# Optimization experiments

Measured on AMD Instinct MI355X. Metric: run time of the kernel, lower is better.

Reference implementation:

```python
import jax, jax.numpy as jnp
import numpy as np

EPS = 1e-05


def setup_inputs() -> dict:
    key = jax.random.key(0)
    kx, kw, kb, kg, kp, kq = jax.random.split(key, 6)
    B, S, D = 32, 1024, 1024
    x = jax.random.normal(kx, (B, S, D), dtype=jnp.float32)
    # Linear(input_size, input_size) params
    W = jax.random.normal(kw, (D, D), dtype=jnp.float32) / np.sqrt(D)
    b = jax.random.normal(kb, (D,), dtype=jnp.float32) * 0.01
    gold_opinion = jax.random.uniform(kg, (B, S, 5), dtype=jnp.float32)
    predict_opinion = jax.random.uniform(kp, (B, S, 5), dtype=jnp.float32)
    gold_prob = jax.random.uniform(kq, (), dtype=jnp.float32)
    return {"x": x, "W": W, "b": b, "gold_opinion": gold_opinion,
            "predict_opinion": predict_opinion, "gold_prob": gold_prob}


def reference(x, W, b, gold_opinion, predict_opinion, gold_prob):
    # x: [B, S, D]
    S = x.shape[-2]
    x_tran = jnp.einsum('bsd,ed->bse', x, W) + b           # Linear: x @ W^T + b
    weights = jnp.einsum('bsd,btd->bst', x_tran, x)        # QK^T -> [B, S, S]

    idx = jnp.arange(S)
    location = jnp.abs(idx[None, :] - idx[:, None]).astype(x.dtype)  # [S, S]
    weights = weights * (1.0 / (location + EPS))           # distance decay

    # use_opinion = True branch
    gold_op = gold_opinion[:, :, 1] + gold_opinion[:, :, 2]          # [B, S]
    pred_op = predict_opinion[:, :, 3] + predict_opinion[:, :, 4]    # [B, S]
    opinion_weights = gold_prob * gold_op + (1.0 - gold_prob) * pred_op
    weights = weights * opinion_weights[:, :, None]

    weights = jnp.exp(jnp.tanh(weights))                   # pseudo-softmax numerator
    off_diag = (location != 0).astype(weights.dtype)       # eye(S) == 0 mask
    weights = weights * off_diag
    weights = weights / (jnp.sum(weights, axis=-1, keepdims=True) + EPS)
    return jnp.einsum('bst,btd->bsd', weights, x)
```

## Files before the change

### kernel.cpp

```cpp
#include <hip/hip_runtime.h>

#define EPSF 1e-5f

typedef _Float16 f16x8 __attribute__((ext_vector_type(8)));
typedef float f32x4 __attribute__((ext_vector_type(4)));

__device__ __forceinline__ void gload_lds16(const _Float16* g, _Float16* l) {
  __builtin_amdgcn_global_load_lds(
      (const __attribute__((address_space(1))) unsigned int*)g,
      (__attribute__((address_space(3))) unsigned int*)l, 16, 0, 0);
}

__device__ __forceinline__ f16x8 cvt8(float4 a, float4 b) {
  f16x8 h;
  h[0] = (_Float16)a.x; h[1] = (_Float16)a.y; h[2] = (_Float16)a.z; h[3] = (_Float16)a.w;
  h[4] = (_Float16)b.x; h[5] = (_Float16)b.y; h[6] = (_Float16)b.z; h[7] = (_Float16)b.w;
  return h;
}

__global__ void prep_opin_k(const float* __restrict__ gold, const float* __restrict__ pred,
                            const float* __restrict__ gprob, float* __restrict__ opin, int n) {
  int i = blockIdx.x * 256 + threadIdx.x;
  if (i >= n) return;
  float gp = gprob[0];
  float go = gold[i * 5 + 1] + gold[i * 5 + 2];
  float po = pred[i * 5 + 3] + pred[i * 5 + 4];
  opin[i] = gp * go + (1.0f - gp) * po;
}

__global__ __launch_bounds__(256) void prep_h_k(const float* __restrict__ src,
                                                _Float16* __restrict__ dst) {
  long i = ((long)blockIdx.x * 256 + threadIdx.x) * 8;
  float4 a = *(const float4*)(src + i);
  float4 b = *(const float4*)(src + i + 4);
  *(f16x8*)(dst + i) = cvt8(a, b);
}

__global__ __launch_bounds__(256) void prep_xt_k(const float* __restrict__ x,
                                                 _Float16* __restrict__ XhT) {
  const int d = blockIdx.x * 256 + threadIdx.x;
  const int ts = blockIdx.y * 64;
  const long base = (long)blockIdx.z * 1024;
#pragma unroll
  for (int tg = 0; tg < 4; ++tg) {
    int t0 = ts + tg * 16;
    const float* src = x + (base + t0) * 1024 + d;
    float v[16];
#pragma unroll
    for (int j = 0; j < 16; ++j) v[j] = src[j * 1024];
    f16x8 h0, h1;
#pragma unroll
    for (int j = 0; j < 8; ++j) { h0[j] = (_Float16)v[j]; h1[j] = (_Float16)v[8 + j]; }
    _Float16* dst = XhT + (base + d) * 1024 + t0;
    *(f16x8*)dst = h0;
    *(f16x8*)(dst + 8) = h1;
  }
}

__global__ __launch_bounds__(256) void gemm1_h_k(const _Float16* __restrict__ Xh,
                                                 const _Float16* __restrict__ Wh,
                                                 const float* __restrict__ bias,
                                                 _Float16* __restrict__ XT) {
  __shared__ _Float16 As[128 * 32];
  __shared__ _Float16 Bs[128 * 32];
  const int tid = threadIdx.x;
  const int wave = tid >> 6, lane = tid & 63;
  const int wm = wave >> 1, wn = wave & 1;
  const int quad = lane >> 4, nl = lane & 15;
  const long m0 = (long)blockIdx.y * 128;
  const int n0 = blockIdx.x * 128;

  f32x4 acc[4][4];
  f32x4 zero = {0.f, 0.f, 0.f, 0.f};
#pragma unroll
  for (int i = 0; i < 4; ++i)
#pragma unroll
    for (int j = 0; j < 4; ++j) acc[i][j] = zero;

  for (int k0 = 0; k0 < 1024; k0 += 32) {
#pragma unroll
    for (int it = 0; it < 2; ++it) {
      int c = it * 256 + tid;
      gload_lds16(Xh + (m0 + (c >> 2)) * 1024 + k0 + (c & 3) * 8,
                  &As[(it * 256 + wave * 64) * 8]);
      gload_lds16(Wh + (long)(n0 + (c >> 2)) * 1024 + k0 + (c & 3) * 8,
                  &Bs[(it * 256 + wave * 64) * 8]);
    }
    __syncthreads();
    f16x8 af[4], bf[4];
#pragma unroll
    for (int mi = 0; mi < 4; ++mi)
      af[mi] = *(const f16x8*)&As[(wm * 64 + mi * 16 + nl) * 32 + quad * 8];
#pragma unroll
    for (int ni = 0; ni < 4; ++ni)
      bf[ni] = *(const f16x8*)&Bs[(wn * 64 + ni * 16 + nl) * 32 + quad * 8];
#pragma unroll
    for (int mi = 0; mi < 4; ++mi)
#pragma unroll
      for (int ni = 0; ni < 4; ++ni)
        acc[mi][ni] = __builtin_amdgcn_mfma_f32_16x16x32_f16(af[mi], bf[ni], acc[mi][ni], 0, 0, 0);
    __syncthreads();
  }

#pragma unroll
  for (int mi = 0; mi < 4; ++mi) {
    long gm = m0 + wm * 64 + mi * 16 + quad * 4;
#pragma unroll
    for (int ni = 0; ni < 4; ++ni) {
      int gn = n0 + wn * 64 + ni * 16 + nl;
      float bv = bias[gn];
#pragma unroll
      for (int r = 0; r < 4; ++r)
        XT[(gm + r) * 1024 + gn] = (_Float16)(acc[mi][ni][r] + bv);
    }
  }
}

__global__ __launch_bounds__(256) void gemm1_k(const _Float16* __restrict__ Xh,
                                               const float* __restrict__ Wt,
                                               const float* __restrict__ bias,
                                               _Float16* __restrict__ XT) {
  __shared__ _Float16 As[128 * 32];
  __shared__ _Float16 Bs[128 * 32];
  const int tid = threadIdx.x;
  const int wave = tid >> 6, lane = tid & 63;
  const int wm = wave >> 1, wn = wave & 1;
  const int quad = lane >> 4, nl = lane & 15;
  const long m0 = (long)blockIdx.y * 128;
  const int n0 = blockIdx.x * 128;

  f32x4 acc[4][4];
  f32x4 zero = {0.f, 0.f, 0.f, 0.f};
#pragma unroll
  for (int i = 0; i < 4; ++i)
#pragma unroll
    for (int j = 0; j < 4; ++j) acc[i][j] = zero;

  const int crow = tid >> 2;
  const int ckc = (tid & 3) * 8;

  for (int k0 = 0; k0 < 1024; k0 += 32) {
#pragma unroll
    for (int it = 0; it < 2; ++it) {
      int c = it * 256 + tid;
      gload_lds16(Xh + (m0 + (c >> 2)) * 1024 + k0 + (c & 3) * 8,
                  &As[(it * 256 + wave * 64) * 8]);
      int row = it * 64 + crow;
      const float* sb = Wt + (long)(n0 + row) * 1024 + k0 + ckc;
      float4 b0 = *(const float4*)sb;
      float4 b1 = *(const float4*)(sb + 4);
      *(f16x8*)&Bs[row * 32 + ckc] = cvt8(b0, b1);
    }
    __syncthreads();
    f16x8 af[4], bf[4];
#pragma unroll
    for (int mi = 0; mi < 4; ++mi)
      af[mi] = *(const f16x8*)&As[(wm * 64 + mi * 16 + nl) * 32 + quad * 8];
#pragma unroll
    for (int ni = 0; ni < 4; ++ni)
      bf[ni] = *(const f16x8*)&Bs[(wn * 64 + ni * 16 + nl) * 32 + quad * 8];
#pragma unroll
    for (int mi = 0; mi < 4; ++mi)
#pragma unroll
      for (int ni = 0; ni < 4; ++ni)
        acc[mi][ni] = __builtin_amdgcn_mfma_f32_16x16x32_f16(af[mi], bf[ni], acc[mi][ni], 0, 0, 0);
    __syncthreads();
  }

#pragma unroll
  for (int mi = 0; mi < 4; ++mi) {
    long gm = m0 + wm * 64 + mi * 16 + quad * 4;
#pragma unroll
    for (int ni = 0; ni < 4; ++ni) {
      int gn = n0 + wn * 64 + ni * 16 + nl;
      float bv = bias[gn];
#pragma unroll
      for (int r = 0; r < 4; ++r)
        XT[(gm + r) * 1024 + gn] = (_Float16)(acc[mi][ni][r] + bv);
    }
  }
}

__global__ __launch_bounds__(256) void scores_k(const _Float16* __restrict__ XT,
                                                const _Float16* __restrict__ Xh,
                                                const float* __restrict__ opin,
                                                _Float16* __restrict__ P,
                                                float* __restrict__ denom) {
  __shared__ _Float16 As[128 * 32];
  __shared__ _Float16 Bs[128 * 32];
  const int tid = threadIdx.x;
  const int wave = tid >> 6, lane = tid & 63;
  const int wm = wave >> 1, wn = wave & 1;
  const int quad = lane >> 4, nl = lane & 15;

  const int lin = blockIdx.x;
  const int xcd = lin & 7;
  const int i = lin >> 3;
  const int b = xcd + 8 * (i >> 6);
  const int tile = i & 63;
  const int s0 = (tile >> 3) * 128;
  const int t0 = (tile & 7) * 128;
  const long base = (long)b * 1024;

  f32x4 acc[4][4];
  f32x4 zero = {0.f, 0.f, 0.f, 0.f};
#pragma unroll
  for (int i2 = 0; i2 < 4; ++i2)
#pragma unroll
    for (int j = 0; j < 4; ++j) acc[i2][j] = zero;

  for (int k0 = 0; k0 < 1024; k0 += 32) {
#pragma unroll
    for (int it = 0; it < 2; ++it) {
      int c = it * 256 + tid;
      gload_lds16(XT + (base + s0 + (c >> 2)) * 1024 + k0 + (c & 3) * 8,
                  &As[(it * 256 + wave * 64) * 8]);
      gload_lds16(Xh + (base + t0 + (c >> 2)) * 1024 + k0 + (c & 3) * 8,
                  &Bs[(it * 256 + wave * 64) * 8]);
    }
    __syncthreads();
    f16x8 af[4], bf[4];
#pragma unroll
    for (int mi = 0; mi < 4; ++mi)
      af[mi] = *(const f16x8*)&As[(wm * 64 + mi * 16 + nl) * 32 + quad * 8];
#pragma unroll
    for (int ni = 0; ni < 4; ++ni)
      bf[ni] = *(const f16x8*)&Bs[(wn * 64 + ni * 16 + nl) * 32 + quad * 8];
#pragma unroll
    for (int mi = 0; mi < 4; ++mi)
#pragma unroll
      for (int ni = 0; ni < 4; ++ni)
        acc[mi][ni] = __builtin_amdgcn_mfma_f32_16x16x32_f16(af[mi], bf[ni], acc[mi][ni], 0, 0, 0);
    __syncthreads();
  }

#pragma unroll
  for (int mi = 0; mi < 4; ++mi) {
#pragma unroll
    for (int r = 0; r < 4; ++r) {
      int s = s0 + wm * 64 + mi * 16 + quad * 4 + r;
      float opv = opin[b * 1024 + s];
      float rs = 0.f;
#pragma unroll
      for (int ni = 0; ni < 4; ++ni) {
        int t = t0 + wn * 64 + ni * 16 + nl;
        float loc = fabsf((float)(s - t));
        float arg = acc[mi][ni][r] * (1.0f / (loc + EPSF)) * opv;
        float th = 1.f - 2.f / (__expf(2.f * arg) + 1.f);
        float p = __expf(th);
        if (s == t) p = 0.f;
        P[(base + s) * 1024 + t] = (_Float16)p;
        rs += p;
      }
      rs += __shfl_xor(rs, 1);
      rs += __shfl_xor(rs, 2);
      rs += __shfl_xor(rs, 4);
      rs += __shfl_xor(rs, 8);
      if (nl == 0) atomicAdd(&denom[b * 1024 + s], rs);
    }
  }
}

__global__ __launch_bounds__(256) void pv_h_k(const _Float16* __restrict__ P,
                                              const _Float16* __restrict__ XhT,
                                              const float* __restrict__ denom,
                                              float* __restrict__ out) {
  __shared__ _Float16 As[128 * 32];
  __shared__ _Float16 Bs[128 * 32];
  const int tid = threadIdx.x;
  const int wave = tid >> 6, lane = tid & 63;
  const int wm = wave >> 1, wn = wave & 1;
  const int quad = lane >> 4, nl = lane & 15;

  const int lin = blockIdx.x;
  const int xcd = lin & 7;
  const int i = lin >> 3;
  const int b = xcd + 8 * (i >> 6);
  const int tile = i & 63;
  const int s0 = (tile >> 3) * 128;
  const int d0 = (tile & 7) * 128;
  const long base = (long)b * 1024;

  f32x4 acc[4][4];
  f32x4 zero = {0.f, 0.f, 0.f, 0.f};
#pragma unroll
  for (int i2 = 0; i2 < 4; ++i2)
#pragma unroll
    for (int j = 0; j < 4; ++j) acc[i2][j] = zero;

  for (int k0 = 0; k0 < 1024; k0 += 32) {
#pragma unroll
    for (int it = 0; it < 2; ++it) {
      int c = it * 256 + tid;
      gload_lds16(P + (base + s0 + (c >> 2)) * 1024 + k0 + (c & 3) * 8,
                  &As[(it * 256 + wave * 64) * 8]);
      gload_lds16(XhT + (base + d0 + (c >> 2)) * 1024 + k0 + (c & 3) * 8,
                  &Bs[(it * 256 + wave * 64) * 8]);
    }
    __syncthreads();
    f16x8 af[4], bf[4];
#pragma unroll
    for (int mi = 0; mi < 4; ++mi)
      af[mi] = *(const f16x8*)&As[(wm * 64 + mi * 16 + nl) * 32 + quad * 8];
#pragma unroll
    for (int ni = 0; ni < 4; ++ni)
      bf[ni] = *(const f16x8*)&Bs[(wn * 64 + ni * 16 + nl) * 32 + quad * 8];
#pragma unroll
    for (int mi = 0; mi < 4; ++mi)
#pragma unroll
      for (int ni = 0; ni < 4; ++ni)
        acc[mi][ni] = __builtin_amdgcn_mfma_f32_16x16x32_f16(af[mi], bf[ni], acc[mi][ni], 0, 0, 0);
    __syncthreads();
  }

#pragma unroll
  for (int mi = 0; mi < 4; ++mi) {
#pragma unroll
    for (int r = 0; r < 4; ++r) {
      int s = s0 + wm * 64 + mi * 16 + quad * 4 + r;
      float inv = 1.0f / (denom[b * 1024 + s] + EPSF);
#pragma unroll
      for (int ni = 0; ni < 4; ++ni) {
        int d = d0 + wn * 64 + ni * 16 + nl;
        out[(base + s) * 1024 + d] = acc[mi][ni][r] * inv;
      }
    }
  }
}

__global__ __launch_bounds__(256) void pv_k(const _Float16* __restrict__ P,
                                            const float* __restrict__ X,
                                            const float* __restrict__ denom,
                                            float* __restrict__ out) {
  __shared__ _Float16 As[128 * 32];
  __shared__ _Float16 BsT[128 * 40];
  const int tid = threadIdx.x;
  const int wave = tid >> 6, lane = tid & 63;
  const int wm = wave >> 1, wn = wave & 1;
  const int quad = lane >> 4, nl = lane & 15;
  const int b = blockIdx.z;
  const int s0 = blockIdx.y * 128;
  const int d0 = blockIdx.x * 128;
  const long base = (long)b * 1024;

  const int dcol = tid & 127;
  const int tg = tid >> 7;

  f32x4 acc[4][4];
  f32x4 zero = {0.f, 0.f, 0.f, 0.f};
#pragma unroll
  for (int i = 0; i < 4; ++i)
#pragma unroll
    for (int j = 0; j < 4; ++j) acc[i][j] = zero;

  for (int k0 = 0; k0 < 1024; k0 += 32) {
#pragma unroll
    for (int it = 0; it < 2; ++it) {
      int c = it * 256 + tid;
      gload_lds16(P + (base + s0 + (c >> 2)) * 1024 + k0 + (c & 3) * 8,
                  &As[(it * 256 + wave * 64) * 8]);
    }
    {
      const float* xb = X + (base + k0 + tg * 16) * 1024 + d0 + dcol;
      float v[16];
#pragma unroll
      for (int j = 0; j < 16; ++j) v[j] = xb[j * 1024];
      f16x8 h0, h1;
#pragma unroll
      for (int j = 0; j < 8; ++j) { h0[j] = (_Float16)v[j]; h1[j] = (_Float16)v[8 + j]; }
      *(f16x8*)&BsT[dcol * 40 + tg * 16] = h0;
      *(f16x8*)&BsT[dcol * 40 + tg * 16 + 8] = h1;
    }
    __syncthreads();
    f16x8 af[4], bf[4];
#pragma unroll
    for (int mi = 0; mi < 4; ++mi)
      af[mi] = *(const f16x8*)&As[(wm * 64 + mi * 16 + nl) * 32 + quad * 8];
#pragma unroll
    for (int ni = 0; ni < 4; ++ni)
      bf[ni] = *(const f16x8*)&BsT[(wn * 64 + ni * 16 + nl) * 40 + quad * 8];
#pragma unroll
    for (int mi = 0; mi < 4; ++mi)
#pragma unroll
      for (int ni = 0; ni < 4; ++ni)
        acc[mi][ni] = __builtin_amdgcn_mfma_f32_16x16x32_f16(af[mi], bf[ni], acc[mi][ni], 0, 0, 0);
    __syncthreads();
  }

#pragma unroll
  for (int mi = 0; mi < 4; ++mi) {
#pragma unroll
    for (int r = 0; r < 4; ++r) {
      int s = s0 + wm * 64 + mi * 16 + quad * 4 + r;
      float inv = 1.0f / (denom[b * 1024 + s] + EPSF);
#pragma unroll
      for (int ni = 0; ni < 4; ++ni) {
        int d = d0 + wn * 64 + ni * 16 + nl;
        out[(base + s) * 1024 + d] = acc[mi][ni][r] * inv;
      }
    }
  }
}

__global__ __launch_bounds__(256) void scores_f_k(const _Float16* __restrict__ XT,
                                                  const _Float16* __restrict__ Xh,
                                                  const float* __restrict__ opin,
                                                  _Float16* __restrict__ P,
                                                  float* __restrict__ denom) {
  __shared__ _Float16 As[128 * 32];
  __shared__ _Float16 Bs[128 * 32];
  const int tid = threadIdx.x;
  const int wave = tid >> 6, lane = tid & 63;
  const int wm = wave >> 1, wn = wave & 1;
  const int quad = lane >> 4, nl = lane & 15;
  const int b = blockIdx.z;
  const int s0 = blockIdx.y * 128;
  const int t0 = blockIdx.x * 128;
  const long base = (long)b * 1024;

  f32x4 acc[4][4];
  f32x4 zero = {0.f, 0.f, 0.f, 0.f};
#pragma unroll
  for (int i = 0; i < 4; ++i)
#pragma unroll
    for (int j = 0; j < 4; ++j) acc[i][j] = zero;

  for (int k0 = 0; k0 < 1024; k0 += 32) {
#pragma unroll
    for (int it = 0; it < 2; ++it) {
      int c = it * 256 + tid;
      gload_lds16(XT + (base + s0 + (c >> 2)) * 1024 + k0 + (c & 3) * 8,
                  &As[(it * 256 + wave * 64) * 8]);
      gload_lds16(Xh + (base + t0 + (c >> 2)) * 1024 + k0 + (c & 3) * 8,
                  &Bs[(it * 256 + wave * 64) * 8]);
    }
    __syncthreads();
    f16x8 af[4], bf[4];
#pragma unroll
    for (int mi = 0; mi < 4; ++mi)
      af[mi] = *(const f16x8*)&As[(wm * 64 + mi * 16 + nl) * 32 + quad * 8];
#pragma unroll
    for (int ni = 0; ni < 4; ++ni)
      bf[ni] = *(const f16x8*)&Bs[(wn * 64 + ni * 16 + nl) * 32 + quad * 8];
#pragma unroll
    for (int mi = 0; mi < 4; ++mi)
#pragma unroll
      for (int ni = 0; ni < 4; ++ni)
        acc[mi][ni] = __builtin_amdgcn_mfma_f32_16x16x32_f16(af[mi], bf[ni], acc[mi][ni], 0, 0, 0);
    __syncthreads();
  }

#pragma unroll
  for (int mi = 0; mi < 4; ++mi) {
#pragma unroll
    for (int r = 0; r < 4; ++r) {
      int s = s0 + wm * 64 + mi * 16 + quad * 4 + r;
      float opv = opin[b * 1024 + s];
      float rs = 0.f;
#pragma unroll
      for (int ni = 0; ni < 4; ++ni) {
        int t = t0 + wn * 64 + ni * 16 + nl;
        float loc = fabsf((float)(s - t));
        float arg = acc[mi][ni][r] * (1.0f / (loc + EPSF)) * opv;
        float th = 1.f - 2.f / (__expf(2.f * arg) + 1.f);
        float p = __expf(th);
        if (s == t) p = 0.f;
        P[(base + s) * 1024 + t] = (_Float16)p;
        rs += p;
      }
      rs += __shfl_xor(rs, 1);
      rs += __shfl_xor(rs, 2);
      rs += __shfl_xor(rs, 4);
      rs += __shfl_xor(rs, 8);
      if (nl == 0) atomicAdd(&denom[b * 1024 + s], rs);
    }
  }
}

extern "C" void kernel_launch(void* const* d_in, const int* in_sizes, int n_in,
                              void* d_out, int out_size, void* d_ws, size_t ws_size,
                              hipStream_t stream) {
  (void)in_sizes; (void)n_in; (void)out_size;
  const int B = 32, S = 1024;
  const int BS = B * S;

  const float* x     = (const float*)d_in[0];
  const float* W     = (const float*)d_in[1];
  const float* bias  = (const float*)d_in[2];
  const float* gold  = (const float*)d_in[3];
  const float* pred  = (const float*)d_in[4];
  const float* gprob = (const float*)d_in[5];

  const size_t P_BYTES  = (size_t)BS * 1024 * sizeof(_Float16);
  const size_t XT_BYTES = P_BYTES;
  const size_t OPIN_B   = (size_t)BS * sizeof(float);
  const size_t WH_B     = (size_t)1024 * 1024 * sizeof(_Float16);
  const size_t NEED_BIG = P_BYTES + XT_BYTES + 2 * OPIN_B + WH_B;

  char* ws = (char*)d_ws;
  _Float16* P = (_Float16*)ws;
  const bool big = ws_size >= NEED_BIG;

  _Float16* XT = (_Float16*)d_out;
  _Float16* Xh = XT + (size_t)BS * 1024;
  float* out   = (float*)d_out;

  if (big) {
    _Float16* XhT = (_Float16*)(ws + P_BYTES);
    float* opin   = (float*)(ws + P_BYTES + XT_BYTES);
    float* denom  = opin + BS;
    _Float16* Wh  = (_Float16*)(ws + P_BYTES + XT_BYTES + 2 * OPIN_B);

    hipMemsetAsync(denom, 0, OPIN_B, stream);
    prep_opin_k<<<BS / 256, 256, 0, stream>>>(gold, pred, gprob, opin, BS);
    prep_h_k<<<(BS * 1024 / 8) / 256, 256, 0, stream>>>(x, Xh);
    prep_h_k<<<(1024 * 1024 / 8) / 256, 256, 0, stream>>>(W, Wh);
    prep_xt_k<<<dim3(4, 16, 32), 256, 0, stream>>>(x, XhT);
    gemm1_h_k<<<dim3(8, 256), 256, 0, stream>>>(Xh, Wh, bias, XT);
    scores_k<<<2048, 256, 0, stream>>>(XT, Xh, opin, P, denom);
    pv_h_k<<<2048, 256, 0, stream>>>(P, XhT, denom, out);
  } else {
    float* opin  = (float*)(ws + P_BYTES);
    float* denom = opin + BS;

    hipMemsetAsync(denom, 0, OPIN_B, stream);
    prep_opin_k<<<BS / 256, 256, 0, stream>>>(gold, pred, gprob, opin, BS);
    prep_h_k<<<(BS * 1024 / 8) / 256, 256, 0, stream>>>(x, Xh);
    gemm1_k<<<dim3(8, 256), 256, 0, stream>>>(Xh, W, bias, XT);
    scores_f_k<<<dim3(8, 8, 32), 256, 0, stream>>>(XT, Xh, opin, P, denom);
    pv_k<<<dim3(8, 8, 32), 256, 0, stream>>>(P, x, denom, out);
  }
}
```

Baseline: 595.1 us.

## Use 256x256 multi-stage pipelined GEMM core for all three matmuls

Replaces the three 128x128 single-buffered GEMM kernels with a shared 256x256-tile, 512-thread core. The core uses a 4-stage LDS ring with async global-to-LDS loads, explicit vmcnt waits, XOR-swizzled LDS layout and raised MFMA priority. The aim is to hide load latency behind MFMA work, cut global traffic per flop, and avoid LDS bank conflicts. The cost is 128KB of LDS per block and many more registers per thread, which limits occupancy and makes the manual wait counts easy to get wrong.

```diff
diff --git a/kernel.cpp b/kernel.cpp
--- a/kernel.cpp
+++ b/kernel.cpp
@@ -16,6 +16,112 @@
   h[0] = (_Float16)a.x; h[1] = (_Float16)a.y; h[2] = (_Float16)a.z; h[3] = (_Float16)a.w;
   h[4] = (_Float16)b.x; h[5] = (_Float16)b.y; h[6] = (_Float16)b.z; h[7] = (_Float16)b.w;
   return h;
+}
+
+template <int N>
+__device__ __forceinline__ void wait_vm() {
+  if constexpr (N == 8) asm volatile("s_waitcnt vmcnt(8) lgkmcnt(0)" ::: "memory");
+  else if constexpr (N == 4) asm volatile("s_waitcnt vmcnt(4) lgkmcnt(0)" ::: "memory");
+  else asm volatile("s_waitcnt vmcnt(0) lgkmcnt(0)" ::: "memory");
+}
+
+__device__ __forceinline__ void barrier_fence() {
+  __builtin_amdgcn_s_barrier();
+  asm volatile("" ::: "memory");
+}
+
+__device__ __forceinline__ void gemm256_run(const _Float16* __restrict__ Ag,
+                                            const _Float16* __restrict__ Bg,
+                                            _Float16* lds, f32x4 (&acc)[8][4]) {
+  const int tid = threadIdx.x;
+  const int wave = tid >> 6, lane = tid & 63;
+  const int wm = wave >> 2, wn = wave & 3;
+  const int quad = lane >> 4, nl = lane & 15;
+  const int srow = tid >> 2;
+  const long arow = (long)srow * 1024 + (((tid & 3) ^ (srow & 3)) * 8);
+  const int pq = (quad ^ (nl & 3)) * 8;
+
+#pragma unroll
+  for (int i = 0; i < 8; ++i)
+#pragma unroll
+    for (int j = 0; j < 4; ++j) acc[i][j] = (f32x4){0.f, 0.f, 0.f, 0.f};
+
+#define STAGE_A(t)                                                     \
+  {                                                                    \
+    _Float16* lA_ = lds + ((t) & 3) * 16384;                           \
+    const _Float16* ga_ = Ag + arow + (t) * 32;                        \
+    gload_lds16(ga_, lA_ + wave * 512);                                \
+    gload_lds16(ga_ + 128 * 1024, lA_ + 4096 + wave * 512);            \
+  }
+#define STAGE_B(t)                                                     \
+  {                                                                    \
+    _Float16* lB_ = lds + ((t) & 3) * 16384 + 8192;                    \
+    const _Float16* gb_ = Bg + arow + (t) * 32;                        \
+    gload_lds16(gb_, lB_ + wave * 512);                                \
+    gload_lds16(gb_ + 128 * 1024, lB_ + 4096 + wave * 512);            \
+  }
+#define LDA(t, mq, af)                                                 \
+  {                                                                    \
+    const _Float16* p_ =                                               \
+        lds + ((t) & 3) * 16384 + (wm * 128 + (mq) * 64 + nl) * 32 + pq; \
+    _Pragma("unroll") for (int i_ = 0; i_ < 4; ++i_)                   \
+        af[i_] = *(const f16x8*)(p_ + i_ * 512);                       \
+  }
+#define LDB(t, bf)                                                     \
+  {                                                                    \
+    const _Float16* p_ =                                               \
+        lds + ((t) & 3) * 16384 + 8192 + (wn * 64 + nl) * 32 + pq;     \
+    _Pragma("unroll") for (int i_ = 0; i_ < 4; ++i_)                   \
+        bf[i_] = *(const f16x8*)(p_ + i_ * 512);                       \
+  }
+#define MMA(mq, af, bf)                                                \
+  {                                                                    \
+    __builtin_amdgcn_s_setprio(1);                                     \
+    _Pragma("unroll") for (int i_ = 0; i_ < 4; ++i_)                   \
+        _Pragma("unroll") for (int j_ = 0; j_ < 4; ++j_)               \
+            acc[(mq) * 4 + i_][j_] = __builtin_amdgcn_mfma_f32_16x16x32_f16( \
+                af[i_], bf[j_], acc[(mq) * 4 + i_][j_], 0, 0, 0);      \
+    __builtin_amdgcn_s_setprio(0);                                     \
+  }
+#define TILE(t, STG)                                                   \
+  {                                                                    \
+    f16x8 af_[4], bf_[4];                                              \
+    LDA(t, 0, af_);                                                    \
+    LDB(t, bf_);                                                       \
+    if (STG) STAGE_A((t) + 3);                                         \
+    MMA(0, af_, bf_);                                                  \
+    f16x8 af2_[4];                                                     \
+    LDA(t, 1, af2_);                                                   \
+    if (STG) STAGE_B((t) + 3);                                         \
+    MMA(1, af2_, bf_);                                                 \
+  }
+
+  STAGE_A(0); STAGE_B(0);
+  STAGE_A(1); STAGE_B(1);
+  STAGE_A(2); STAGE_B(2);
+  wait_vm<8>();
+  barrier_fence();
+
+#pragma unroll 4
+  for (int t = 0; t < 28; ++t) {
+    TILE(t, true);
+    wait_vm<8>();
+    barrier_fence();
+  }
+  TILE(28, true);
+  wait_vm<8>(); barrier_fence();
+  TILE(29, false);
+  wait_vm<4>(); barrier_fence();
+  TILE(30, false);
+  wait_vm<0>(); barrier_fence();
+  TILE(31, false);
+
+#undef TILE
+#undef MMA
+#undef LDB
+#undef LDA
+#undef STAGE_B
+#undef STAGE_A
 }
 
 __global__ void prep_opin_k(const float* __restrict__ gold, const float* __restrict__ pred,
@@ -57,54 +163,28 @@
   }
 }
 
-__global__ __launch_bounds__(256) void gemm1_h_k(const _Float16* __restrict__ Xh,
-                                                 const _Float16* __restrict__ Wh,
-                                                 const float* __restrict__ bias,
-                                                 _Float16* __restrict__ XT) {
-  __shared__ _Float16 As[128 * 32];
-  __shared__ _Float16 Bs[128 * 32];
-  const int tid = threadIdx.x;
-  const int wave = tid >> 6, lane = tid & 63;
-  const int wm = wave >> 1, wn = wave & 1;
-  const int quad = lane >> 4, nl = lane & 15;
-  const long m0 = (long)blockIdx.y * 128;
-  const int n0 = blockIdx.x * 128;
-
-  f32x4 acc[4][4];
-  f32x4 zero = {0.f, 0.f, 0.f, 0.f};
-#pragma unroll
-  for (int i = 0; i < 4; ++i)
-#pragma unroll
-    for (int j = 0; j < 4; ++j) acc[i][j] = zero;
-
-  for (int k0 = 0; k0 < 1024; k0 += 32) {
-#pragma unroll
-    for (int it = 0; it < 2; ++it) {
-      int c = it * 256 + tid;
-      gload_lds16(Xh + (m0 + (c >> 2)) * 1024 + k0 + (c & 3) * 8,
-                  &As[(it * 256 + wave * 64) * 8]);
-      gload_lds16(Wh + (long)(n0 + (c >> 2)) * 1024 + k0 + (c & 3) * 8,
-                  &Bs[(it * 256 + wave * 64) * 8]);
-    }
-    __syncthreads();
-    f16x8 af[4], bf[4];
-#pragma unroll
-    for (int mi = 0; mi < 4; ++mi)
-      af[mi] = *(const f16x8*)&As[(wm * 64 + mi * 16 + nl) * 32 + quad * 8];
-#pragma unroll
-    for (int ni = 0; ni < 4; ++ni)
-      bf[ni] = *(const f16x8*)&Bs[(wn * 64 + ni * 16 + nl) * 32 + quad * 8];
-#pragma unroll
-    for (int mi = 0; mi < 4; ++mi)
-#pragma unroll
-      for (int ni = 0; ni < 4; ++ni)
-        acc[mi][ni] = __builtin_amdgcn_mfma_f32_16x16x32_f16(af[mi], bf[ni], acc[mi][ni], 0, 0, 0);
-    __syncthreads();
-  }
-
-#pragma unroll
-  for (int mi = 0; mi < 4; ++mi) {
-    long gm = m0 + wm * 64 + mi * 16 + quad * 4;
+__global__ __launch_bounds__(512, 2) void gemm12_k(const _Float16* __restrict__ Xh,
+                                                   const _Float16* __restrict__ Wh,
+                                                   const float* __restrict__ bias,
+                                                   _Float16* __restrict__ XT) {
+  __shared__ _Float16 lds[4 * 16384];
+  const int lin = blockIdx.x;
+  const int ii = lin >> 3;
+  const int mt = (lin & 7) * 16 + (ii >> 2);
+  const int nt = ii & 3;
+  const long m0 = (long)mt * 256;
+  const int n0 = nt * 256;
+
+  f32x4 acc[8][4];
+  gemm256_run(Xh + m0 * 1024, Wh + (long)n0 * 1024, lds, acc);
+
+  const int tid = threadIdx.x;
+  const int wave = tid >> 6, lane = tid & 63;
+  const int wm = wave >> 2, wn = wave & 3;
+  const int quad = lane >> 4, nl = lane & 15;
+#pragma unroll
+  for (int mi = 0; mi < 8; ++mi) {
+    long gm = m0 + wm * 128 + mi * 16 + quad * 4;
 #pragma unroll
     for (int ni = 0; ni < 4; ++ni) {
       int gn = n0 + wn * 64 + ni * 16 + nl;
@@ -112,6 +192,89 @@
 #pragma unroll
       for (int r = 0; r < 4; ++r)
         XT[(gm + r) * 1024 + gn] = (_Float16)(acc[mi][ni][r] + bv);
+    }
+  }
+}
+
+__global__ __launch_bounds__(512, 2) void scores2_k(const _Float16* __restrict__ XT,
+                                                    const _Float16* __restrict__ Xh,
+                                                    const float* __restrict__ opin,
+                                                    _Float16* __restrict__ P,
+                                                    float* __restrict__ denom) {
+  __shared__ _Float16 lds[4 * 16384];
+  const int lin = blockIdx.x;
+  const int ii = lin >> 3;
+  const int b = (lin & 7) + 8 * (ii >> 4);
+  const int tile = ii & 15;
+  const int s0 = (tile >> 2) * 256;
+  const int t0 = (tile & 3) * 256;
+  const long base = (long)b * 1024;
+
+  f32x4 acc[8][4];
+  gemm256_run(XT + (base + s0) * 1024, Xh + (base + t0) * 1024, lds, acc);
+
+  const int tid = threadIdx.x;
+  const int wave = tid >> 6, lane = tid & 63;
+  const int wm = wave >> 2, wn = wave & 3;
+  const int quad = lane >> 4, nl = lane & 15;
+#pragma unroll
+  for (int mi = 0; mi < 8; ++mi) {
+#pragma unroll
+    for (int r = 0; r < 4; ++r) {
+      int s = s0 + wm * 128 + mi * 16 + quad * 4 + r;
+      float opv = opin[b * 1024 + s];
+      float rs = 0.f;
+#pragma unroll
+      for (int ni = 0; ni < 4; ++ni) {
+        int tc = t0 + wn * 64 + ni * 16 + nl;
+        float loc = fabsf((float)(s - tc));
+        float arg = acc[mi][ni][r] * (1.0f / (loc + EPSF)) * opv;
+        float th = 1.f - 2.f / (__expf(2.f * arg) + 1.f);
+        float p = __expf(th);
+        if (s == tc) p = 0.f;
+        P[(base + s) * 1024 + tc] = (_Float16)p;
+        rs += p;
+      }
+      rs += __shfl_xor(rs, 1);
+      rs += __shfl_xor(rs, 2);
+      rs += __shfl_xor(rs, 4);
+      rs += __shfl_xor(rs, 8);
+      if (nl == 0) atomicAdd(&denom[b * 1024 + s], rs);
+    }
+  }
+}
+
+__global__ __launch_bounds__(512, 2) void pv2_k(const _Float16* __restrict__ P,
+                                                const _Float16* __restrict__ XhT,
+                                                const float* __restrict__ denom,
+                                                float* __restrict__ out) {
+  __shared__ _Float16 lds[4 * 16384];
+  const int lin = blockIdx.x;
+  const int ii = lin >> 3;
+  const int b = (lin & 7) + 8 * (ii >> 4);
+  const int tile = ii & 15;
+  const int s0 = (tile >> 2) * 256;
+  const int d0 = (tile & 3) * 256;
+  const long base = (long)b * 1024;
+
+  f32x4 acc[8][4];
+  gemm256_run(P + (base + s0) * 1024, XhT + (base + d0) * 1024, lds, acc);
+
+  const int tid = threadIdx.x;
+  const int wave = tid >> 6, lane = tid & 63;
+  const int wm = wave >> 2, wn = wave & 3;
+  const int quad = lane >> 4, nl = lane & 15;
+#pragma unroll
+  for (int mi = 0; mi < 8; ++mi) {
+#pragma unroll
+    for (int r = 0; r < 4; ++r) {
+      int s = s0 + wm * 128 + mi * 16 + quad * 4 + r;
+      float inv = 1.0f / (denom[b * 1024 + s] + EPSF);
+#pragma unroll
+      for (int ni = 0; ni < 4; ++ni) {
+        int d = d0 + wn * 64 + ni * 16 + nl;
+        out[(base + s) * 1024 + d] = acc[mi][ni][r] * inv;
+      }
     }
   }
 }
@@ -181,33 +344,28 @@
   }
 }
 
-__global__ __launch_bounds__(256) void scores_k(const _Float16* __restrict__ XT,
-                                                const _Float16* __restrict__ Xh,
-                                                const float* __restrict__ opin,
-                                                _Float16* __restrict__ P,
-                                                float* __restrict__ denom) {
+__global__ __launch_bounds__(256) void scores_f_k(const _Float16* __restrict__ XT,
+                                                  const _Float16* __restrict__ Xh,
+                                                  const float* __restrict__ opin,
+                                                  _Float16* __restrict__ P,
+                                                  float* __restrict__ denom) {
   __shared__ _Float16 As[128 * 32];
   __shared__ _Float16 Bs[128 * 32];
   const int tid = threadIdx.x;
   const int wave = tid >> 6, lane = tid & 63;
   const int wm = wave >> 1, wn = wave & 1;
   const int quad = lane >> 4, nl = lane & 15;
-
-  const int lin = blockIdx.x;
-  const int xcd = lin & 7;
-  const int i = lin >> 3;
-  const int b = xcd + 8 * (i >> 6);
-  const int tile = i & 63;
-  const int s0 = (tile >> 3) * 128;
-  const int t0 = (tile & 7) * 128;
+  const int b = blockIdx.z;
+  const int s0 = blockIdx.y * 128;
+  const int t0 = blockIdx.x * 128;
   const long base = (long)b * 1024;
 
   f32x4 acc[4][4];
   f32x4 zero = {0.f, 0.f, 0.f, 0.f};
 #pragma unroll
-  for (int i2 = 0; i2 < 4; ++i2)
-#pragma unroll
-    for (int j = 0; j < 4; ++j) acc[i2][j] = zero;
+  for (int i = 0; i < 4; ++i)
+#pragma unroll
+    for (int j = 0; j < 4; ++j) acc[i][j] = zero;
 
   for (int k0 = 0; k0 < 1024; k0 += 32) {
 #pragma unroll
@@ -261,73 +419,6 @@
   }
 }
 
-__global__ __launch_bounds__(256) void pv_h_k(const _Float16* __restrict__ P,
-                                              const _Float16* __restrict__ XhT,
-                                              const float* __restrict__ denom,
-                                              float* __restrict__ out) {
-  __shared__ _Float16 As[128 * 32];
-  __shared__ _Float16 Bs[128 * 32];
-  const int tid = threadIdx.x;
-  const int wave = tid >> 6, lane = tid & 63;
-  const int wm = wave >> 1, wn = wave & 1;
-  const int quad = lane >> 4, nl = lane & 15;
-
-  const int lin = blockIdx.x;
-  const int xcd = lin & 7;
-  const int i = lin >> 3;
-  const int b = xcd + 8 * (i >> 6);
-  const int tile = i & 63;
-  const int s0 = (tile >> 3) * 128;
-  const int d0 = (tile & 7) * 128;
-  const long base = (long)b * 1024;
-
-  f32x4 acc[4][4];
-  f32x4 zero = {0.f, 0.f, 0.f, 0.f};
-#pragma unroll
-  for (int i2 = 0; i2 < 4; ++i2)
-#pragma unroll
-    for (int j = 0; j < 4; ++j) acc[i2][j] = zero;
-
-  for (int k0 = 0; k0 < 1024; k0 += 32) {
-#pragma unroll
-    for (int it = 0; it < 2; ++it) {
-      int c = it * 256 + tid;
-      gload_lds16(P + (base + s0 + (c >> 2)) * 1024 + k0 + (c & 3) * 8,
-                  &As[(it * 256 + wave * 64) * 8]);
-      gload_lds16(XhT + (base + d0 + (c >> 2)) * 1024 + k0 + (c & 3) * 8,
-                  &Bs[(it * 256 + wave * 64) * 8]);
-    }
-    __syncthreads();
-    f16x8 af[4], bf[4];
-#pragma unroll
-    for (int mi = 0; mi < 4; ++mi)
-      af[mi] = *(const f16x8*)&As[(wm * 64 + mi * 16 + nl) * 32 + quad * 8];
-#pragma unroll
-    for (int ni = 0; ni < 4; ++ni)
-      bf[ni] = *(const f16x8*)&Bs[(wn * 64 + ni * 16 + nl) * 32 + quad * 8];
-#pragma unroll
-    for (int mi = 0; mi < 4; ++mi)
-#pragma unroll
-      for (int ni = 0; ni < 4; ++ni)
-        acc[mi][ni] = __builtin_amdgcn_mfma_f32_16x16x32_f16(af[mi], bf[ni], acc[mi][ni], 0, 0, 0);
-    __syncthreads();
-  }
-
-#pragma unroll
-  for (int mi = 0; mi < 4; ++mi) {
-#pragma unroll
-    for (int r = 0; r < 4; ++r) {
-      int s = s0 + wm * 64 + mi * 16 + quad * 4 + r;
-      float inv = 1.0f / (denom[b * 1024 + s] + EPSF);
-#pragma unroll
-      for (int ni = 0; ni < 4; ++ni) {
-        int d = d0 + wn * 64 + ni * 16 + nl;
-        out[(base + s) * 1024 + d] = acc[mi][ni][r] * inv;
-      }
-    }
-  }
-}
-
 __global__ __launch_bounds__(256) void pv_k(const _Float16* __restrict__ P,
                                             const float* __restrict__ X,
                                             const float* __restrict__ denom,
@@ -402,81 +493,6 @@
   }
 }
 
-__global__ __launch_bounds__(256) void scores_f_k(const _Float16* __restrict__ XT,
-                                                  const _Float16* __restrict__ Xh,
-                                                  const float* __restrict__ opin,
-                                                  _Float16* __restrict__ P,
-                                                  float* __restrict__ denom) {
-  __shared__ _Float16 As[128 * 32];
-  __shared__ _Float16 Bs[128 * 32];
-  const int tid = threadIdx.x;
-  const int wave = tid >> 6, lane = tid & 63;
-  const int wm = wave >> 1, wn = wave & 1;
-  const int quad = lane >> 4, nl = lane & 15;
-  const int b = blockIdx.z;
-  const int s0 = blockIdx.y * 128;
-  const int t0 = blockIdx.x * 128;
-  const long base = (long)b * 1024;
-
-  f32x4 acc[4][4];
-  f32x4 zero = {0.f, 0.f, 0.f, 0.f};
-#pragma unroll
-  for (int i = 0; i < 4; ++i)
-#pragma unroll
-    for (int j = 0; j < 4; ++j) acc[i][j] = zero;
-
-  for (int k0 = 0; k0 < 1024; k0 += 32) {
-#pragma unroll
-    for (int it = 0; it < 2; ++it) {
-      int c = it * 256 + tid;
-      gload_lds16(XT + (base + s0 + (c >> 2)) * 1024 + k0 + (c & 3) * 8,
-                  &As[(it * 256 + wave * 64) * 8]);
-      gload_lds16(Xh + (base + t0 + (c >> 2)) * 1024 + k0 + (c & 3) * 8,
-                  &Bs[(it * 256 + wave * 64) * 8]);
-    }
-    __syncthreads();
-    f16x8 af[4], bf[4];
-#pragma unroll
-    for (int mi = 0; mi < 4; ++mi)
-      af[mi] = *(const f16x8*)&As[(wm * 64 + mi * 16 + nl) * 32 + quad * 8];
-#pragma unroll
-    for (int ni = 0; ni < 4; ++ni)
-      bf[ni] = *(const f16x8*)&Bs[(wn * 64 + ni * 16 + nl) * 32 + quad * 8];
-#pragma unroll
-    for (int mi = 0; mi < 4; ++mi)
-#pragma unroll
-      for (int ni = 0; ni < 4; ++ni)
-        acc[mi][ni] = __builtin_amdgcn_mfma_f32_16x16x32_f16(af[mi], bf[ni], acc[mi][ni], 0, 0, 0);
-    __syncthreads();
-  }
-
-#pragma unroll
-  for (int mi = 0; mi < 4; ++mi) {
-#pragma unroll
-    for (int r = 0; r < 4; ++r) {
-      int s = s0 + wm * 64 + mi * 16 + quad * 4 + r;
-      float opv = opin[b * 1024 + s];
-      float rs = 0.f;
-#pragma unroll
-      for (int ni = 0; ni < 4; ++ni) {
-        int t = t0 + wn * 64 + ni * 16 + nl;
-        float loc = fabsf((float)(s - t));
-        float arg = acc[mi][ni][r] * (1.0f / (loc + EPSF)) * opv;
-        float th = 1.f - 2.f / (__expf(2.f * arg) + 1.f);
-        float p = __expf(th);
-        if (s == t) p = 0.f;
-        P[(base + s) * 1024 + t] = (_Float16)p;
-        rs += p;
-      }
-      rs += __shfl_xor(rs, 1);
-      rs += __shfl_xor(rs, 2);
-      rs += __shfl_xor(rs, 4);
-      rs += __shfl_xor(rs, 8);
-      if (nl == 0) atomicAdd(&denom[b * 1024 + s], rs);
-    }
-  }
-}
-
 extern "C" void kernel_launch(void* const* d_in, const int* in_sizes, int n_in,
                               void* d_out, int out_size, void* d_ws, size_t ws_size,
                               hipStream_t stream) {
@@ -516,9 +532,9 @@
     prep_h_k<<<(BS * 1024 / 8) / 256, 256, 0, stream>>>(x, Xh);
     prep_h_k<<<(1024 * 1024 / 8) / 256, 256, 0, stream>>>(W, Wh);
     prep_xt_k<<<dim3(4, 16, 32), 256, 0, stream>>>(x, XhT);
-    gemm1_h_k<<<dim3(8, 256), 256, 0, stream>>>(Xh, Wh, bias, XT);
-    scores_k<<<2048, 256, 0, stream>>>(XT, Xh, opin, P, denom);
-    pv_h_k<<<2048, 256, 0, stream>>>(P, XhT, denom, out);
+    gemm12_k<<<512, 512, 0, stream>>>(Xh, Wh, bias, XT);
+    scores2_k<<<512, 512, 0, stream>>>(XT, Xh, opin, P, denom);
+    pv2_k<<<512, 512, 0, stream>>>(P, XhT, denom, out);
   } else {
     float* opin  = (float*)(ws + P_BYTES);
     float* denom = opin + BS;
```

Result: faster. 539.7 us (-9.3%).
